# Kernel optimization log

Measured on AMD Instinct MI355X. Metric: run time of the kernel, lower is better.

Reference implementation:

```python
import jax, jax.numpy as jnp
import numpy as np

NUM_HEADS = 12


def setup_inputs() -> dict:
    key = jax.random.key(0)
    k1, k2, k3 = jax.random.split(key, 3)
    B, N, D = 16, 1024, 768
    x = jax.random.normal(k1, (B, N, D), dtype=jnp.float32)
    qkv_w = jax.random.normal(k2, (D, 3 * D), dtype=jnp.float32) * (1.0 / np.sqrt(D))
    proj_w = jax.random.normal(k3, (D, D), dtype=jnp.float32) * (1.0 / np.sqrt(D))
    proj_b = jnp.zeros((D,), dtype=jnp.float32)
    return {"x": x, "qkv_w": qkv_w, "proj_w": proj_w, "proj_b": proj_b}


def reference(x, qkv_w, proj_w, proj_b):
    B, N, D = x.shape
    H = NUM_HEADS
    hd = D // H
    scale = hd ** -0.5
    qkv = jnp.einsum('bnd,de->bne', x, qkv_w)
    qkv = qkv.reshape(B, N, 3, H, hd).transpose(2, 0, 3, 1, 4)
    q, k, v = qkv[0], qkv[1], qkv[2]
    # attention scores [B, H, N, N]
    attn = jnp.einsum('bhqd,bhkd->bhqk', q, k) * scale
    attn = jax.nn.softmax(attn, axis=-1)
    out = jnp.einsum('bhqk,bhkd->bhqd', attn, v)
    out = out.transpose(0, 2, 1, 3).reshape(B, N, D)
    # output projection
    return jnp.einsum('bnd,de->bne', out, proj_w) + proj_b
```

## Files before the change

### kernel.cpp

```cpp
#include <hip/hip_runtime.h>
#include <cstdint>
#include <cstddef>

typedef float f32x4 __attribute__((ext_vector_type(4)));
typedef __bf16 bf16x8 __attribute__((ext_vector_type(8)));

#define BB 16
#define SEQ 1024
#define DMODEL 768
#define NHEAD 12
#define HDIM 64
#define MTOT (BB * SEQ)
#define NQKV (3 * DMODEL)
#define NQK (2 * DMODEL)
#define QSCALE 0.18033688011112042f

static __device__ __forceinline__ unsigned short f2bf(float f) {
  unsigned int u = __builtin_bit_cast(unsigned int, f);
  u += 0x7fffu + ((u >> 16) & 1u);
  return (unsigned short)(u >> 16);
}

static __device__ __forceinline__ unsigned cvt_pk_bf16(float lo, float hi) {
  unsigned r;
  asm("v_cvt_pk_bf16_f32 %0, %1, %2" : "=v"(r) : "v"(lo), "v"(hi));
  return r;
}

static __device__ __forceinline__ float max3f(float a, float b, float c) {
  return fmaxf(fmaxf(a, b), c);
}

static __device__ __forceinline__ void gload_lds16(const void* g, void* l) {
  __builtin_amdgcn_global_load_lds((__attribute__((address_space(1))) void*)g,
                                   (__attribute__((address_space(3))) void*)l,
                                   16, 0, 0);
}

__global__ __launch_bounds__(256) void k_prep(
    const float4* __restrict__ x4, ushort4* __restrict__ xb4,
    const float* __restrict__ qkv_w, unsigned short* __restrict__ WqT,
    const float* __restrict__ proj_w, unsigned short* __restrict__ WpT) {
  const int blk = blockIdx.x;
  if (blk < 1024) {
    const int n4 = MTOT * DMODEL / 4;
    const int stride = 1024 * 256;
    for (int i = blk * 256 + threadIdx.x; i < n4; i += stride) {
      float4 v = x4[i];
      ushort4 o;
      o.x = f2bf(v.x); o.y = f2bf(v.y); o.z = f2bf(v.z); o.w = f2bf(v.w);
      xb4[i] = o;
    }
    return;
  }
  __shared__ float tile[32][33];
  const float* in; unsigned short* out; int C, scaleN, bx, by;
  if (blk < 1024 + 1728) {
    const int l = blk - 1024; bx = l % 72; by = l / 72;
    in = qkv_w; out = WqT; C = NQKV; scaleN = DMODEL;
  } else {
    const int l = blk - 2752; bx = l % 24; by = l / 24;
    in = proj_w; out = WpT; C = DMODEL; scaleN = 0;
  }
  const int R = DMODEL;
  const int tx = threadIdx.x & 31, ty = threadIdx.x >> 5;
  const int c0 = bx * 32, r0 = by * 32;
#pragma unroll
  for (int i = 0; i < 4; ++i)
    tile[ty + i * 8][tx] = in[(size_t)(r0 + ty + i * 8) * C + c0 + tx];
  __syncthreads();
#pragma unroll
  for (int i = 0; i < 4; ++i) {
    const int n = c0 + ty + i * 8;
    float v = tile[tx][ty + i * 8];
    if (n < scaleN) v *= QSCALE;
    out[(size_t)n * R + r0 + tx] = f2bf(v);
  }
}

template <int MODE>
__global__ __launch_bounds__(256, 4) void k_gemm_bt(
    const unsigned short* __restrict__ A, const unsigned short* __restrict__ Bt,
    int M, int N, int K,
    float* __restrict__ outF, const float* __restrict__ bias,
    unsigned short* __restrict__ QK, unsigned short* __restrict__ Vt) {
  __shared__ __align__(16) unsigned short As[128 * 64];
  __shared__ __align__(16) unsigned short Bs[128 * 64];
  const int tid = threadIdx.x;
  const int lane = tid & 63, wid = tid >> 6;
  const int ln15 = lane & 15, lh = lane >> 4;
  const int wr = wid >> 1, wc = wid & 1;
  const int m0 = blockIdx.x * 128, n0 = blockIdx.y * 128;
  f32x4 acc[4][4] = {};
  const int srow = lane >> 3;
  const int sblk = ((lane & 7) ^ srow) * 8;
  const int swz = (ln15 & 7) << 3;
  const int nk = K >> 6;

  for (int kt = 0; kt < nk; ++kt) {
    const int k0 = kt * 64;
#pragma unroll
    for (int c = 0; c < 4; ++c) {
      const int ch = wid * 4 + c;
      const int row = ch * 8 + srow;
      gload_lds16(A + (size_t)(m0 + row) * K + k0 + sblk, &As[ch * 512]);
      gload_lds16(Bt + (size_t)(n0 + row) * K + k0 + sblk, &Bs[ch * 512]);
    }
    __syncthreads();
#pragma unroll
    for (int kk = 0; kk < 2; ++kk) {
      const int kc = kk * 32 + lh * 8;
      bf16x8 af[4], bfv[4];
#pragma unroll
      for (int mt = 0; mt < 4; ++mt)
        af[mt] = *reinterpret_cast<const bf16x8*>(
            &As[(wr * 64 + mt * 16 + ln15) * 64 + (kc ^ swz)]);
#pragma unroll
      for (int nn = 0; nn < 4; ++nn)
        bfv[nn] = *reinterpret_cast<const bf16x8*>(
            &Bs[(wc * 64 + nn * 16 + ln15) * 64 + (kc ^ swz)]);
#pragma unroll
      for (int mt = 0; mt < 4; ++mt)
#pragma unroll
        for (int nn = 0; nn < 4; ++nn)
          acc[mt][nn] = __builtin_amdgcn_mfma_f32_16x16x32_bf16(af[mt], bfv[nn], acc[mt][nn], 0, 0, 0);
    }
    __syncthreads();
  }

#pragma unroll
  for (int mt = 0; mt < 4; ++mt) {
#pragma unroll
    for (int nn = 0; nn < 4; ++nn) {
      const int nb = n0 + wc * 64 + nn * 16;
      const int mb = m0 + wr * 64 + mt * 16 + lh * 4;
      if (MODE == 0) {
#pragma unroll
        for (int r = 0; r < 4; ++r)
          outF[(size_t)(mb + r) * N + nb + ln15] = acc[mt][nn][r] + bias[nb + ln15];
      } else if (nb < NQK) {
#pragma unroll
        for (int r = 0; r < 4; ++r)
          QK[(size_t)(mb + r) * NQK + nb + ln15] = f2bf(acc[mt][nn][r]);
      } else {
        const int rr = nb + ln15 - NQK;
        const int h = rr >> 6, d = rr & 63;
        const int b = mb >> 10, nr0 = mb & 1023;
        ushort4 u;
        u.x = f2bf(acc[mt][nn][0]); u.y = f2bf(acc[mt][nn][1]);
        u.z = f2bf(acc[mt][nn][2]); u.w = f2bf(acc[mt][nn][3]);
        *reinterpret_cast<ushort4*>(
            &Vt[(((size_t)b * NHEAD + h) * HDIM + d) * SEQ + nr0]) = u;
      }
    }
  }
}

__global__ __launch_bounds__(512) void k_attn(
    const unsigned short* __restrict__ QKn, const unsigned short* __restrict__ Vt,
    unsigned short* __restrict__ O) {
  __shared__ __align__(16) unsigned short Ks[64 * 64];
  __shared__ __align__(16) unsigned short Vs[64 * 64];
  __shared__ __align__(16) unsigned short Ps[8][16 * 72];
  const int tid = threadIdx.x;
  const int lane = tid & 63, w = tid >> 6;
  const int ln15 = lane & 15, lh = lane >> 4;
  const int o = blockIdx.x;
  const int sid = (o & 7) * 192 + (o >> 3);
  const int qb = sid & 7;
  const int bhid = sid >> 3;
  const int h = bhid % NHEAD;
  const int b = bhid / NHEAD;
  const size_t bh = (size_t)(b * NHEAD + h);
  const unsigned short* Qbase = QKn + (size_t)(b * SEQ + qb * 128 + w * 16) * NQK + h * HDIM;
  const unsigned short* Kbase = QKn + (size_t)(b * SEQ) * NQK + DMODEL + h * HDIM;
  const unsigned short* Vbase = Vt + bh * HDIM * SEQ;

  const int srow = lane >> 3;
  const int sblk = ((lane & 7) ^ srow) * 8;
  const int swz = (ln15 & 7) << 3;

  bf16x8 aq[2];
#pragma unroll
  for (int ch = 0; ch < 2; ++ch)
    aq[ch] = *reinterpret_cast<const bf16x8*>(Qbase + (size_t)ln15 * NQK + ch * 32 + lh * 8);

  bf16x8 onesb;
#pragma unroll
  for (int i = 0; i < 8; ++i) onesb[i] = (__bf16)1.0f;

  f32x4 acc[4] = {};
  f32x4 accl = {};
  float mr = 0.f;
  f32x4 cinit = {};

  for (int kb = 0; kb < SEQ / 64; ++kb) {
    {
      const int row = w * 8 + srow;
      gload_lds16(Kbase + (size_t)(kb * 64 + row) * NQK + sblk, &Ks[w * 512]);
      gload_lds16(Vbase + (size_t)row * SEQ + kb * 64 + sblk, &Vs[w * 512]);
    }
    __syncthreads();

    f32x4 sv[4];
#pragma unroll
    for (int t = 0; t < 4; ++t) sv[t] = cinit;
    __builtin_amdgcn_s_setprio(1);
#pragma unroll
    for (int t = 0; t < 4; ++t) {
#pragma unroll
      for (int ch = 0; ch < 2; ++ch) {
        bf16x8 bk = *reinterpret_cast<const bf16x8*>(
            &Ks[(t * 16 + ln15) * 64 + ((ch * 32 + lh * 8) ^ swz)]);
        sv[t] = __builtin_amdgcn_mfma_f32_16x16x32_bf16(bk, aq[ch], sv[t], 0, 0, 0);
      }
    }
    __builtin_amdgcn_s_setprio(0);

    float pm;
    {
      const float g0 = max3f(sv[0][0], sv[0][1], sv[0][2]);
      const float g1 = max3f(sv[0][3], sv[1][0], sv[1][1]);
      const float g2 = max3f(sv[1][2], sv[1][3], sv[2][0]);
      const float g3 = max3f(sv[2][1], sv[2][2], sv[2][3]);
      const float g4 = max3f(sv[3][0], sv[3][1], sv[3][2]);
      pm = fmaxf(max3f(g0, g1, g2), max3f(g3, g4, sv[3][3]));
    }
    if (__any(pm > 8.f)) {
      float bmf = pm;
      bmf = fmaxf(bmf, __shfl_xor(bmf, 16));
      bmf = fmaxf(bmf, __shfl_xor(bmf, 32));
      const float delta = fmaxf(bmf, 0.f);
      const float al = __builtin_amdgcn_exp2f(-delta);
#pragma unroll
      for (int t = 0; t < 4; ++t)
#pragma unroll
        for (int r = 0; r < 4; ++r) sv[t][r] -= delta;
      mr += delta;
      cinit[0] = -mr; cinit[1] = -mr; cinit[2] = -mr; cinit[3] = -mr;
      float alq[4];
#pragma unroll
      for (int r = 0; r < 4; ++r) alq[r] = __shfl(al, lh * 4 + r);
#pragma unroll
      for (int dt = 0; dt < 4; ++dt)
#pragma unroll
        for (int r = 0; r < 4; ++r) acc[dt][r] *= alq[r];
#pragma unroll
      for (int r = 0; r < 4; ++r) accl[r] *= alq[r];
    }

#pragma unroll
    for (int t = 0; t < 4; ++t)
#pragma unroll
      for (int r = 0; r < 4; ++r) sv[t][r] = __builtin_amdgcn_exp2f(sv[t][r]);

#pragma unroll
    for (int t = 0; t < 4; ++t) {
      uint2 u;
      u.x = cvt_pk_bf16(sv[t][0], sv[t][1]);
      u.y = cvt_pk_bf16(sv[t][2], sv[t][3]);
      *reinterpret_cast<uint2*>(&Ps[w][ln15 * 72 + t * 16 + lh * 4]) = u;
    }

    bf16x8 ap[2];
#pragma unroll
    for (int ch = 0; ch < 2; ++ch)
      ap[ch] = *reinterpret_cast<const bf16x8*>(&Ps[w][ln15 * 72 + ch * 32 + lh * 8]);
    __builtin_amdgcn_s_setprio(1);
#pragma unroll
    for (int ch = 0; ch < 2; ++ch)
      accl = __builtin_amdgcn_mfma_f32_16x16x32_bf16(ap[ch], onesb, accl, 0, 0, 0);
#pragma unroll
    for (int dt = 0; dt < 4; ++dt) {
#pragma unroll
      for (int ch = 0; ch < 2; ++ch) {
        bf16x8 bv = *reinterpret_cast<const bf16x8*>(
            &Vs[(dt * 16 + ln15) * 64 + ((ch * 32 + lh * 8) ^ swz)]);
        acc[dt] = __builtin_amdgcn_mfma_f32_16x16x32_bf16(ap[ch], bv, acc[dt], 0, 0, 0);
      }
    }
    __builtin_amdgcn_s_setprio(0);
    __syncthreads();
  }

  const int qrow = qb * 128 + w * 16 + lh * 4;
#pragma unroll
  for (int dt = 0; dt < 4; ++dt)
#pragma unroll
    for (int r = 0; r < 4; ++r)
      O[((size_t)b * SEQ + qrow + r) * DMODEL + h * 64 + dt * 16 + ln15] =
          f2bf(acc[dt][r] / accl[r]);
}

extern "C" void kernel_launch(void* const* d_in, const int* in_sizes, int n_in,
                              void* d_out, int out_size, void* d_ws, size_t ws_size,
                              hipStream_t stream) {
  const float* x      = (const float*)d_in[0];
  const float* qkv_w  = (const float*)d_in[1];
  const float* proj_w = (const float*)d_in[2];
  const float* proj_b = (const float*)d_in[3];
  float* out = (float*)d_out;

  char* ws = (char*)d_ws;
  const size_t SZ_XB   = (size_t)MTOT * DMODEL * 2;
  const size_t SZ_WQT  = (size_t)NQKV * DMODEL * 2;
  const size_t SZ_WPT  = (size_t)DMODEL * DMODEL * 2;
  const size_t SZ_QK   = (size_t)MTOT * NQK * 2;
  const size_t SZ_VT   = (size_t)BB * NHEAD * HDIM * SEQ * 2;
  unsigned short* Xb   = (unsigned short*)ws;
  unsigned short* WqT  = (unsigned short*)(ws + SZ_XB);
  unsigned short* WpT  = (unsigned short*)(ws + SZ_XB + SZ_WQT);
  unsigned short* QKn  = (unsigned short*)(ws + SZ_XB + SZ_WQT + SZ_WPT);
  unsigned short* Vt   = (unsigned short*)(ws + SZ_XB + SZ_WQT + SZ_WPT + SZ_QK);
  if (ws_size < SZ_XB + SZ_WQT + SZ_WPT + SZ_QK + SZ_VT) return;

  k_prep<<<3328, 256, 0, stream>>>((const float4*)x, (ushort4*)Xb,
                                   qkv_w, WqT, proj_w, WpT);
  k_gemm_bt<1><<<dim3(MTOT / 128, NQKV / 128), 256, 0, stream>>>(
      Xb, WqT, MTOT, NQKV, DMODEL, nullptr, nullptr, QKn, Vt);
  k_attn<<<BB * NHEAD * 8, 512, 0, stream>>>(QKn, Vt, Xb);
  k_gemm_bt<0><<<dim3(MTOT / 128, DMODEL / 128), 256, 0, stream>>>(
      Xb, WpT, MTOT, DMODEL, DMODEL, out, proj_b, nullptr, nullptr);
}
```

Baseline: 167.8 us.

## Switch attention kernel to 32x32x16 MFMA with 4 waves of 32 query rows

```diff
diff --git a/kernel.cpp b/kernel.cpp
--- a/kernel.cpp
+++ b/kernel.cpp
@@ -3,6 +3,7 @@
 #include <cstddef>
 
 typedef float f32x4 __attribute__((ext_vector_type(4)));
+typedef float f32x16 __attribute__((ext_vector_type(16)));
 typedef __bf16 bf16x8 __attribute__((ext_vector_type(8)));
 
 #define BB 16
@@ -156,15 +157,15 @@
   }
 }
 
-__global__ __launch_bounds__(512) void k_attn(
+__global__ __launch_bounds__(256, 4) void k_attn(
     const unsigned short* __restrict__ QKn, const unsigned short* __restrict__ Vt,
     unsigned short* __restrict__ O) {
   __shared__ __align__(16) unsigned short Ks[64 * 64];
   __shared__ __align__(16) unsigned short Vs[64 * 64];
-  __shared__ __align__(16) unsigned short Ps[8][16 * 72];
+  __shared__ __align__(16) unsigned short Ps[4][32 * 72];
   const int tid = threadIdx.x;
   const int lane = tid & 63, w = tid >> 6;
-  const int ln15 = lane & 15, lh = lane >> 4;
+  const int ln31 = lane & 31, lh1 = lane >> 5;
   const int o = blockIdx.x;
   const int sid = (o & 7) * 192 + (o >> 3);
   const int qb = sid & 7;
@@ -172,124 +173,134 @@
   const int h = bhid % NHEAD;
   const int b = bhid / NHEAD;
   const size_t bh = (size_t)(b * NHEAD + h);
-  const unsigned short* Qbase = QKn + (size_t)(b * SEQ + qb * 128 + w * 16) * NQK + h * HDIM;
+  const unsigned short* Qrow = QKn + (size_t)(b * SEQ + qb * 128 + w * 32 + ln31) * NQK + h * HDIM;
   const unsigned short* Kbase = QKn + (size_t)(b * SEQ) * NQK + DMODEL + h * HDIM;
   const unsigned short* Vbase = Vt + bh * HDIM * SEQ;
 
   const int srow = lane >> 3;
   const int sblk = ((lane & 7) ^ srow) * 8;
-  const int swz = (ln15 & 7) << 3;
-
-  bf16x8 aq[2];
-#pragma unroll
-  for (int ch = 0; ch < 2; ++ch)
-    aq[ch] = *reinterpret_cast<const bf16x8*>(Qbase + (size_t)ln15 * NQK + ch * 32 + lh * 8);
+  const int rsw = ln31 & 7;
+
+  bf16x8 aq[4];
+#pragma unroll
+  for (int ks = 0; ks < 4; ++ks)
+    aq[ks] = *reinterpret_cast<const bf16x8*>(Qrow + ks * 16 + lh1 * 8);
 
   bf16x8 onesb;
 #pragma unroll
   for (int i = 0; i < 8; ++i) onesb[i] = (__bf16)1.0f;
 
-  f32x4 acc[4] = {};
-  f32x4 accl = {};
+  f32x16 acc0 = {}, acc1 = {};
+  f32x16 accl = {};
   float mr = 0.f;
-  f32x4 cinit = {};
 
   for (int kb = 0; kb < SEQ / 64; ++kb) {
-    {
-      const int row = w * 8 + srow;
-      gload_lds16(Kbase + (size_t)(kb * 64 + row) * NQK + sblk, &Ks[w * 512]);
-      gload_lds16(Vbase + (size_t)row * SEQ + kb * 64 + sblk, &Vs[w * 512]);
+#pragma unroll
+    for (int c = 0; c < 2; ++c) {
+      const int ch = w * 2 + c;
+      const int row = ch * 8 + srow;
+      gload_lds16(Kbase + (size_t)(kb * 64 + row) * NQK + sblk, &Ks[ch * 512]);
+      gload_lds16(Vbase + (size_t)row * SEQ + kb * 64 + sblk, &Vs[ch * 512]);
     }
     __syncthreads();
 
-    f32x4 sv[4];
-#pragma unroll
-    for (int t = 0; t < 4; ++t) sv[t] = cinit;
+    const float nmr = -mr;
+    f32x16 sv0, sv1;
+#pragma unroll
+    for (int i = 0; i < 16; ++i) { sv0[i] = nmr; sv1[i] = nmr; }
     __builtin_amdgcn_s_setprio(1);
 #pragma unroll
-    for (int t = 0; t < 4; ++t) {
-#pragma unroll
-      for (int ch = 0; ch < 2; ++ch) {
-        bf16x8 bk = *reinterpret_cast<const bf16x8*>(
-            &Ks[(t * 16 + ln15) * 64 + ((ch * 32 + lh * 8) ^ swz)]);
-        sv[t] = __builtin_amdgcn_mfma_f32_16x16x32_bf16(bk, aq[ch], sv[t], 0, 0, 0);
-      }
+    for (int ks = 0; ks < 4; ++ks) {
+      const int bo = (((ks * 2 + lh1) ^ rsw) << 3);
+      bf16x8 bk0 = *reinterpret_cast<const bf16x8*>(&Ks[ln31 * 64 + bo]);
+      sv0 = __builtin_amdgcn_mfma_f32_32x32x16_bf16(bk0, aq[ks], sv0, 0, 0, 0);
+      bf16x8 bk1 = *reinterpret_cast<const bf16x8*>(&Ks[(32 + ln31) * 64 + bo]);
+      sv1 = __builtin_amdgcn_mfma_f32_32x32x16_bf16(bk1, aq[ks], sv1, 0, 0, 0);
     }
     __builtin_amdgcn_s_setprio(0);
 
     float pm;
     {
-      const float g0 = max3f(sv[0][0], sv[0][1], sv[0][2]);
-      const float g1 = max3f(sv[0][3], sv[1][0], sv[1][1]);
-      const float g2 = max3f(sv[1][2], sv[1][3], sv[2][0]);
-      const float g3 = max3f(sv[2][1], sv[2][2], sv[2][3]);
-      const float g4 = max3f(sv[3][0], sv[3][1], sv[3][2]);
-      pm = fmaxf(max3f(g0, g1, g2), max3f(g3, g4, sv[3][3]));
+      const float a0 = max3f(sv0[0], sv0[1], sv0[2]);
+      const float a1 = max3f(sv0[3], sv0[4], sv0[5]);
+      const float a2 = max3f(sv0[6], sv0[7], sv0[8]);
+      const float a3 = max3f(sv0[9], sv0[10], sv0[11]);
+      const float a4 = max3f(sv0[12], sv0[13], sv0[14]);
+      const float b0 = max3f(sv0[15], sv1[0], sv1[1]);
+      const float b1 = max3f(sv1[2], sv1[3], sv1[4]);
+      const float b2 = max3f(sv1[5], sv1[6], sv1[7]);
+      const float b3 = max3f(sv1[8], sv1[9], sv1[10]);
+      const float b4 = max3f(sv1[11], sv1[12], sv1[13]);
+      const float c0 = max3f(a0, a1, a2);
+      const float c1 = max3f(a3, a4, b0);
+      const float c2 = max3f(b1, b2, b3);
+      const float c3 = max3f(b4, sv1[14], sv1[15]);
+      pm = fmaxf(fmaxf(c0, c1), fmaxf(c2, c3));
     }
     if (__any(pm > 8.f)) {
-      float bmf = pm;
-      bmf = fmaxf(bmf, __shfl_xor(bmf, 16));
-      bmf = fmaxf(bmf, __shfl_xor(bmf, 32));
+      const float bmf = fmaxf(pm, __shfl_xor(pm, 32));
       const float delta = fmaxf(bmf, 0.f);
       const float al = __builtin_amdgcn_exp2f(-delta);
 #pragma unroll
-      for (int t = 0; t < 4; ++t)
-#pragma unroll
-        for (int r = 0; r < 4; ++r) sv[t][r] -= delta;
+      for (int i = 0; i < 16; ++i) { sv0[i] -= delta; sv1[i] -= delta; }
       mr += delta;
-      cinit[0] = -mr; cinit[1] = -mr; cinit[2] = -mr; cinit[3] = -mr;
-      float alq[4];
-#pragma unroll
-      for (int r = 0; r < 4; ++r) alq[r] = __shfl(al, lh * 4 + r);
-#pragma unroll
-      for (int dt = 0; dt < 4; ++dt)
-#pragma unroll
-        for (int r = 0; r < 4; ++r) acc[dt][r] *= alq[r];
-#pragma unroll
-      for (int r = 0; r < 4; ++r) accl[r] *= alq[r];
-    }
-
-#pragma unroll
-    for (int t = 0; t < 4; ++t)
-#pragma unroll
-      for (int r = 0; r < 4; ++r) sv[t][r] = __builtin_amdgcn_exp2f(sv[t][r]);
-
-#pragma unroll
-    for (int t = 0; t < 4; ++t) {
+      float alq[16];
+#pragma unroll
+      for (int i = 0; i < 16; ++i)
+        alq[i] = __shfl(al, (i & 3) + 8 * (i >> 2) + 4 * lh1);
+#pragma unroll
+      for (int i = 0; i < 16; ++i) {
+        acc0[i] *= alq[i]; acc1[i] *= alq[i]; accl[i] *= alq[i];
+      }
+    }
+
+#pragma unroll
+    for (int i = 0; i < 16; ++i) {
+      sv0[i] = __builtin_amdgcn_exp2f(sv0[i]);
+      sv1[i] = __builtin_amdgcn_exp2f(sv1[i]);
+    }
+
+#pragma unroll
+    for (int g = 0; g < 4; ++g) {
       uint2 u;
-      u.x = cvt_pk_bf16(sv[t][0], sv[t][1]);
-      u.y = cvt_pk_bf16(sv[t][2], sv[t][3]);
-      *reinterpret_cast<uint2*>(&Ps[w][ln15 * 72 + t * 16 + lh * 4]) = u;
-    }
-
-    bf16x8 ap[2];
-#pragma unroll
-    for (int ch = 0; ch < 2; ++ch)
-      ap[ch] = *reinterpret_cast<const bf16x8*>(&Ps[w][ln15 * 72 + ch * 32 + lh * 8]);
+      u.x = cvt_pk_bf16(sv0[g * 4 + 0], sv0[g * 4 + 1]);
+      u.y = cvt_pk_bf16(sv0[g * 4 + 2], sv0[g * 4 + 3]);
+      *reinterpret_cast<uint2*>(&Ps[w][ln31 * 72 + g * 8 + lh1 * 4]) = u;
+      uint2 v;
+      v.x = cvt_pk_bf16(sv1[g * 4 + 0], sv1[g * 4 + 1]);
+      v.y = cvt_pk_bf16(sv1[g * 4 + 2], sv1[g * 4 + 3]);
+      *reinterpret_cast<uint2*>(&Ps[w][ln31 * 72 + 32 + g * 8 + lh1 * 4]) = v;
+    }
+
+    bf16x8 ap[4];
+#pragma unroll
+    for (int ks = 0; ks < 4; ++ks)
+      ap[ks] = *reinterpret_cast<const bf16x8*>(&Ps[w][ln31 * 72 + ks * 16 + lh1 * 8]);
+
     __builtin_amdgcn_s_setprio(1);
 #pragma unroll
-    for (int ch = 0; ch < 2; ++ch)
-      accl = __builtin_amdgcn_mfma_f32_16x16x32_bf16(ap[ch], onesb, accl, 0, 0, 0);
-#pragma unroll
-    for (int dt = 0; dt < 4; ++dt) {
-#pragma unroll
-      for (int ch = 0; ch < 2; ++ch) {
-        bf16x8 bv = *reinterpret_cast<const bf16x8*>(
-            &Vs[(dt * 16 + ln15) * 64 + ((ch * 32 + lh * 8) ^ swz)]);
-        acc[dt] = __builtin_amdgcn_mfma_f32_16x16x32_bf16(ap[ch], bv, acc[dt], 0, 0, 0);
-      }
+    for (int ks = 0; ks < 4; ++ks)
+      accl = __builtin_amdgcn_mfma_f32_32x32x16_bf16(ap[ks], onesb, accl, 0, 0, 0);
+#pragma unroll
+    for (int ks = 0; ks < 4; ++ks) {
+      const int bo = (((ks * 2 + lh1) ^ rsw) << 3);
+      bf16x8 bv0 = *reinterpret_cast<const bf16x8*>(&Vs[ln31 * 64 + bo]);
+      acc0 = __builtin_amdgcn_mfma_f32_32x32x16_bf16(ap[ks], bv0, acc0, 0, 0, 0);
+      bf16x8 bv1 = *reinterpret_cast<const bf16x8*>(&Vs[(32 + ln31) * 64 + bo]);
+      acc1 = __builtin_amdgcn_mfma_f32_32x32x16_bf16(ap[ks], bv1, acc1, 0, 0, 0);
     }
     __builtin_amdgcn_s_setprio(0);
     __syncthreads();
   }
 
-  const int qrow = qb * 128 + w * 16 + lh * 4;
-#pragma unroll
-  for (int dt = 0; dt < 4; ++dt)
-#pragma unroll
-    for (int r = 0; r < 4; ++r)
-      O[((size_t)b * SEQ + qrow + r) * DMODEL + h * 64 + dt * 16 + ln15] =
-          f2bf(acc[dt][r] / accl[r]);
+  const int qg = b * SEQ + qb * 128 + w * 32;
+#pragma unroll
+  for (int i = 0; i < 16; ++i) {
+    const int qrow = (i & 3) + 8 * (i >> 2) + 4 * lh1;
+    const float rl = 1.0f / accl[i];
+    O[(size_t)(qg + qrow) * DMODEL + h * 64 + ln31]      = f2bf(acc0[i] * rl);
+    O[(size_t)(qg + qrow) * DMODEL + h * 64 + 32 + ln31] = f2bf(acc1[i] * rl);
+  }
 }
 
 extern "C" void kernel_launch(void* const* d_in, const int* in_sizes, int n_in,
@@ -318,7 +329,7 @@
                                    qkv_w, WqT, proj_w, WpT);
   k_gemm_bt<1><<<dim3(MTOT / 128, NQKV / 128), 256, 0, stream>>>(
       Xb, WqT, MTOT, NQKV, DMODEL, nullptr, nullptr, QKn, Vt);
-  k_attn<<<BB * NHEAD * 8, 512, 0, stream>>>(QKn, Vt, Xb);
+  k_attn<<<BB * NHEAD * 8, 256, 0, stream>>>(QKn, Vt, Xb);
   k_gemm_bt<0><<<dim3(MTOT / 128, DMODEL / 128), 256, 0, stream>>>(
       Xb, WpT, MTOT, DMODEL, DMODEL, out, proj_b, nullptr, nullptr);
 }
```

Result: slower. 199.8 us (+19.1%).

## Process two query tiles per attention block to reuse K/V tiles

Applied to the files above, without the earlier changes.

```diff
diff --git a/kernel.cpp b/kernel.cpp
--- a/kernel.cpp
+++ b/kernel.cpp
@@ -161,18 +161,17 @@
     unsigned short* __restrict__ O) {
   __shared__ __align__(16) unsigned short Ks[64 * 64];
   __shared__ __align__(16) unsigned short Vs[64 * 64];
-  __shared__ __align__(16) unsigned short Ps[8][16 * 72];
+  __shared__ __align__(16) unsigned short Ps[8][2][16 * 72];
   const int tid = threadIdx.x;
   const int lane = tid & 63, w = tid >> 6;
   const int ln15 = lane & 15, lh = lane >> 4;
   const int o = blockIdx.x;
-  const int sid = (o & 7) * 192 + (o >> 3);
-  const int qb = sid & 7;
-  const int bhid = sid >> 3;
+  const int sid = (o & 7) * 96 + (o >> 3);
+  const int qb = sid & 3;
+  const int bhid = sid >> 2;
   const int h = bhid % NHEAD;
   const int b = bhid / NHEAD;
   const size_t bh = (size_t)(b * NHEAD + h);
-  const unsigned short* Qbase = QKn + (size_t)(b * SEQ + qb * 128 + w * 16) * NQK + h * HDIM;
   const unsigned short* Kbase = QKn + (size_t)(b * SEQ) * NQK + DMODEL + h * HDIM;
   const unsigned short* Vbase = Vt + bh * HDIM * SEQ;
 
@@ -180,19 +179,23 @@
   const int sblk = ((lane & 7) ^ srow) * 8;
   const int swz = (ln15 & 7) << 3;
 
-  bf16x8 aq[2];
-#pragma unroll
-  for (int ch = 0; ch < 2; ++ch)
-    aq[ch] = *reinterpret_cast<const bf16x8*>(Qbase + (size_t)ln15 * NQK + ch * 32 + lh * 8);
+  bf16x8 aq[2][2];
+#pragma unroll
+  for (int tl = 0; tl < 2; ++tl) {
+    const unsigned short* Qb =
+        QKn + (size_t)(b * SEQ + qb * 256 + tl * 128 + w * 16) * NQK + h * HDIM;
+#pragma unroll
+    for (int ch = 0; ch < 2; ++ch)
+      aq[tl][ch] = *reinterpret_cast<const bf16x8*>(Qb + (size_t)ln15 * NQK + ch * 32 + lh * 8);
+  }
 
   bf16x8 onesb;
 #pragma unroll
   for (int i = 0; i < 8; ++i) onesb[i] = (__bf16)1.0f;
 
-  f32x4 acc[4] = {};
-  f32x4 accl = {};
-  float mr = 0.f;
-  f32x4 cinit = {};
+  f32x4 acc[2][4] = {};
+  f32x4 accl[2] = {};
+  float mr[2] = {0.f, 0.f};
 
   for (int kb = 0; kb < SEQ / 64; ++kb) {
     {
@@ -202,94 +205,105 @@
     }
     __syncthreads();
 
-    f32x4 sv[4];
-#pragma unroll
-    for (int t = 0; t < 4; ++t) sv[t] = cinit;
+#pragma unroll
+    for (int tl = 0; tl < 2; ++tl) {
+      const float nmr = -mr[tl];
+      f32x4 sv[4];
+#pragma unroll
+      for (int t = 0; t < 4; ++t) { sv[t][0] = nmr; sv[t][1] = nmr; sv[t][2] = nmr; sv[t][3] = nmr; }
+      __builtin_amdgcn_s_setprio(1);
+#pragma unroll
+      for (int t = 0; t < 4; ++t) {
+#pragma unroll
+        for (int ch = 0; ch < 2; ++ch) {
+          bf16x8 bk = *reinterpret_cast<const bf16x8*>(
+              &Ks[(t * 16 + ln15) * 64 + ((ch * 32 + lh * 8) ^ swz)]);
+          sv[t] = __builtin_amdgcn_mfma_f32_16x16x32_bf16(bk, aq[tl][ch], sv[t], 0, 0, 0);
+        }
+      }
+      __builtin_amdgcn_s_setprio(0);
+
+      float pm;
+      {
+        const float g0 = max3f(sv[0][0], sv[0][1], sv[0][2]);
+        const float g1 = max3f(sv[0][3], sv[1][0], sv[1][1]);
+        const float g2 = max3f(sv[1][2], sv[1][3], sv[2][0]);
+        const float g3 = max3f(sv[2][1], sv[2][2], sv[2][3]);
+        const float g4 = max3f(sv[3][0], sv[3][1], sv[3][2]);
+        pm = fmaxf(max3f(g0, g1, g2), max3f(g3, g4, sv[3][3]));
+      }
+      if (__any(pm > 8.f)) {
+        float bmf = pm;
+        bmf = fmaxf(bmf, __shfl_xor(bmf, 16));
+        bmf = fmaxf(bmf, __shfl_xor(bmf, 32));
+        const float delta = fmaxf(bmf, 0.f);
+        const float al = __builtin_amdgcn_exp2f(-delta);
+#pragma unroll
+        for (int t = 0; t < 4; ++t)
+#pragma unroll
+          for (int r = 0; r < 4; ++r) sv[t][r] -= delta;
+        mr[tl] += delta;
+        float alq[4];
+#pragma unroll
+        for (int r = 0; r < 4; ++r) alq[r] = __shfl(al, lh * 4 + r);
+#pragma unroll
+        for (int dt = 0; dt < 4; ++dt)
+#pragma unroll
+          for (int r = 0; r < 4; ++r) acc[tl][dt][r] *= alq[r];
+#pragma unroll
+        for (int r = 0; r < 4; ++r) accl[tl][r] *= alq[r];
+      }
+
+#pragma unroll
+      for (int t = 0; t < 4; ++t)
+#pragma unroll
+        for (int r = 0; r < 4; ++r) sv[t][r] = __builtin_amdgcn_exp2f(sv[t][r]);
+
+#pragma unroll
+      for (int t = 0; t < 4; ++t) {
+        uint2 u;
+        u.x = cvt_pk_bf16(sv[t][0], sv[t][1]);
+        u.y = cvt_pk_bf16(sv[t][2], sv[t][3]);
+        *reinterpret_cast<uint2*>(&Ps[w][tl][ln15 * 72 + t * 16 + lh * 4]) = u;
+      }
+    }
+
+    bf16x8 ap[2][2];
+#pragma unroll
+    for (int tl = 0; tl < 2; ++tl)
+#pragma unroll
+      for (int ch = 0; ch < 2; ++ch)
+        ap[tl][ch] = *reinterpret_cast<const bf16x8*>(&Ps[w][tl][ln15 * 72 + ch * 32 + lh * 8]);
     __builtin_amdgcn_s_setprio(1);
 #pragma unroll
-    for (int t = 0; t < 4; ++t) {
-#pragma unroll
-      for (int ch = 0; ch < 2; ++ch) {
-        bf16x8 bk = *reinterpret_cast<const bf16x8*>(
-            &Ks[(t * 16 + ln15) * 64 + ((ch * 32 + lh * 8) ^ swz)]);
-        sv[t] = __builtin_amdgcn_mfma_f32_16x16x32_bf16(bk, aq[ch], sv[t], 0, 0, 0);
-      }
-    }
-    __builtin_amdgcn_s_setprio(0);
-
-    float pm;
-    {
-      const float g0 = max3f(sv[0][0], sv[0][1], sv[0][2]);
-      const float g1 = max3f(sv[0][3], sv[1][0], sv[1][1]);
-      const float g2 = max3f(sv[1][2], sv[1][3], sv[2][0]);
-      const float g3 = max3f(sv[2][1], sv[2][2], sv[2][3]);
-      const float g4 = max3f(sv[3][0], sv[3][1], sv[3][2]);
-      pm = fmaxf(max3f(g0, g1, g2), max3f(g3, g4, sv[3][3]));
-    }
-    if (__any(pm > 8.f)) {
-      float bmf = pm;
-      bmf = fmaxf(bmf, __shfl_xor(bmf, 16));
-      bmf = fmaxf(bmf, __shfl_xor(bmf, 32));
-      const float delta = fmaxf(bmf, 0.f);
-      const float al = __builtin_amdgcn_exp2f(-delta);
-#pragma unroll
-      for (int t = 0; t < 4; ++t)
-#pragma unroll
-        for (int r = 0; r < 4; ++r) sv[t][r] -= delta;
-      mr += delta;
-      cinit[0] = -mr; cinit[1] = -mr; cinit[2] = -mr; cinit[3] = -mr;
-      float alq[4];
-#pragma unroll
-      for (int r = 0; r < 4; ++r) alq[r] = __shfl(al, lh * 4 + r);
-#pragma unroll
-      for (int dt = 0; dt < 4; ++dt)
-#pragma unroll
-        for (int r = 0; r < 4; ++r) acc[dt][r] *= alq[r];
-#pragma unroll
-      for (int r = 0; r < 4; ++r) accl[r] *= alq[r];
-    }
-
-#pragma unroll
-    for (int t = 0; t < 4; ++t)
-#pragma unroll
-      for (int r = 0; r < 4; ++r) sv[t][r] = __builtin_amdgcn_exp2f(sv[t][r]);
-
-#pragma unroll
-    for (int t = 0; t < 4; ++t) {
-      uint2 u;
-      u.x = cvt_pk_bf16(sv[t][0], sv[t][1]);
-      u.y = cvt_pk_bf16(sv[t][2], sv[t][3]);
-      *reinterpret_cast<uint2*>(&Ps[w][ln15 * 72 + t * 16 + lh * 4]) = u;
-    }
-
-    bf16x8 ap[2];
-#pragma unroll
-    for (int ch = 0; ch < 2; ++ch)
-      ap[ch] = *reinterpret_cast<const bf16x8*>(&Ps[w][ln15 * 72 + ch * 32 + lh * 8]);
-    __builtin_amdgcn_s_setprio(1);
-#pragma unroll
-    for (int ch = 0; ch < 2; ++ch)
-      accl = __builtin_amdgcn_mfma_f32_16x16x32_bf16(ap[ch], onesb, accl, 0, 0, 0);
+    for (int ch = 0; ch < 2; ++ch) {
+      accl[0] = __builtin_amdgcn_mfma_f32_16x16x32_bf16(ap[0][ch], onesb, accl[0], 0, 0, 0);
+      accl[1] = __builtin_amdgcn_mfma_f32_16x16x32_bf16(ap[1][ch], onesb, accl[1], 0, 0, 0);
+    }
 #pragma unroll
     for (int dt = 0; dt < 4; ++dt) {
 #pragma unroll
       for (int ch = 0; ch < 2; ++ch) {
         bf16x8 bv = *reinterpret_cast<const bf16x8*>(
             &Vs[(dt * 16 + ln15) * 64 + ((ch * 32 + lh * 8) ^ swz)]);
-        acc[dt] = __builtin_amdgcn_mfma_f32_16x16x32_bf16(ap[ch], bv, acc[dt], 0, 0, 0);
+        acc[0][dt] = __builtin_amdgcn_mfma_f32_16x16x32_bf16(ap[0][ch], bv, acc[0][dt], 0, 0, 0);
+        acc[1][dt] = __builtin_amdgcn_mfma_f32_16x16x32_bf16(ap[1][ch], bv, acc[1][dt], 0, 0, 0);
       }
     }
     __builtin_amdgcn_s_setprio(0);
     __syncthreads();
   }
 
-  const int qrow = qb * 128 + w * 16 + lh * 4;
-#pragma unroll
-  for (int dt = 0; dt < 4; ++dt)
-#pragma unroll
-    for (int r = 0; r < 4; ++r)
-      O[((size_t)b * SEQ + qrow + r) * DMODEL + h * 64 + dt * 16 + ln15] =
-          f2bf(acc[dt][r] / accl[r]);
+#pragma unroll
+  for (int tl = 0; tl < 2; ++tl) {
+    const int qrow = qb * 256 + tl * 128 + w * 16 + lh * 4;
+#pragma unroll
+    for (int dt = 0; dt < 4; ++dt)
+#pragma unroll
+      for (int r = 0; r < 4; ++r)
+        O[((size_t)b * SEQ + qrow + r) * DMODEL + h * 64 + dt * 16 + ln15] =
+            f2bf(acc[tl][dt][r] / accl[tl][r]);
+  }
 }
 
 extern "C" void kernel_launch(void* const* d_in, const int* in_sizes, int n_in,
@@ -318,7 +332,7 @@
                                    qkv_w, WqT, proj_w, WpT);
   k_gemm_bt<1><<<dim3(MTOT / 128, NQKV / 128), 256, 0, stream>>>(
       Xb, WqT, MTOT, NQKV, DMODEL, nullptr, nullptr, QKn, Vt);
-  k_attn<<<BB * NHEAD * 8, 512, 0, stream>>>(QKn, Vt, Xb);
+  k_attn<<<BB * NHEAD * 4, 512, 0, stream>>>(QKn, Vt, Xb);
   k_gemm_bt<0><<<dim3(MTOT / 128, DMODEL / 128), 256, 0, stream>>>(
       Xb, WpT, MTOT, DMODEL, DMODEL, out, proj_b, nullptr, nullptr);
 }
```

Result: no change. 167.7 us (-0.1%).
